# Kernel optimization log

Hardware: AMD Instinct MI355X
Metric: run time of the kernel (lower is better)

The kernel has to match this reference:

```python
import jax, jax.numpy as jnp
import numpy as np
import math

# ---- constants lifted verbatim from the torch source ----
PMLX = 10; PX = 400; TX = PMLX + PX + PMLX          # txsize = 420
PMLY = 10; PY = 400; TY = PMLY + PY + PMLY          # tysize = 420
CX = TX // 2; CY = TY // 2
EPS0 = 1e-9 / 36 / math.pi
MU0 = 4 * math.pi * 1e-7
C0 = 1.0 / math.sqrt(MU0 * EPS0)
DX = 2.5e-8; DY = 2.5e-8
DT = 0.99 / C0 / math.sqrt((1.0 / DX) ** 2 + (1.0 / DY) ** 2)
EPSR_INF = 5.283
EPS_INF = EPS0 * EPSR_INF
F0 = 5.47e14; BW = 0.1 * F0
T = math.sqrt(2.0) * math.sqrt(math.log(2.0)) / (math.pi * BW)
NSTEPS = 200   # reduced from 16000 for the correctness baseline; same per-step math


def setup_inputs() -> dict:
    # Lorentz (complex-pole) silver model from param(): pole/residue -> a0,a1,b0,b1,b2
    pr, pi_ = -4.8113e12, 6.8512e13
    rr, ri = 4.9581e14, -1.511e18
    a0 = -2.0 * (pr * rr + pi_ * ri)
    a1 = 2.0 * rr
    b0 = pr * pr + pi_ * pi_
    b1 = -2.0 * pr
    b2 = 1.0
    den = b0 * DT * DT + 2 * b1 * DT + 4 * b2
    Ca = np.array([-(2 * b0 * DT * DT - 8 * b2) / den], np.float32)
    Cb = np.array([-(b0 * DT * DT - 2 * b1 * DT + 4 * b2) / den], np.float32)
    Cc = np.array([(2 * a0 * EPS0 * DT + 4 * a1 * EPS0) / den], np.float32)
    Cd = np.array([-(8 * a1 * EPS0) / den], np.float32)
    Ce = np.array([(-2 * a0 * EPS0 * DT + 4 * a1 * EPS0) / den], np.float32)
    temp1 = float(Cc[0])                       # sum over tot_pol = 1 pole
    denom = EPS_INF / DT + 0.5 * temp1
    C1 = np.full((TX + 1, TY + 1), (EPS_INF / DT) / denom, np.float32)
    C2 = np.full((TX + 1, TY + 1), 0.5 / denom, np.float32)
    Cb_dx = np.full((TX + 1, TY + 1), 1.0 / denom / DX, np.float32)
    Cb_dy = np.full((TX + 1, TY + 1), 1.0 / denom / DY, np.float32)
    dbhx = np.full((TX + 1, TY), DT / MU0 / DY, np.float32)   # Hx curl coeff
    dbhy = np.full((TX, TY + 1), DT / MU0 / DX, np.float32)   # Hy curl coeff
    # polynomial-graded PML conductivity profiles (pml_param)
    m = 4
    eta0 = 120.0 * math.pi
    smax = 0.8 * (m + 1) / (eta0 * DX)

    def prof(n, npml, off):
        k = np.arange(n, dtype=np.float64)
        dl = np.clip(npml - k - off, 0.0, None) / npml   # depth into left PML
        dr = np.clip(k + off - (n - 1 - npml), 0.0, None) / npml
        return (smax * (dl ** m + dr ** m)).astype(np.float32)

    sig_ex = prof(TX + 1, PMLX, 0.0)
    sig_ey = prof(TY + 1, PMLY, 0.0)
    sig_hx = prof(TX, PMLX, 0.5)   # H nodes on half-grid
    sig_hy = prof(TY, PMLY, 0.5)
    # Gaussian-modulated sine soft source at the grid center
    t = np.arange(NSTEPS, dtype=np.float64) * DT
    src = (np.exp(-(((t - 4 * T) / T) ** 2)) * np.sin(2 * math.pi * F0 * (t - 4 * T))).astype(np.float32)
    return {
        "src": jnp.asarray(src), "C1": jnp.asarray(C1), "C2": jnp.asarray(C2),
        "Cb_dx": jnp.asarray(Cb_dx), "Cb_dy": jnp.asarray(Cb_dy),
        "dbhx": jnp.asarray(dbhx), "dbhy": jnp.asarray(dbhy),
        "Ca": jnp.asarray(Ca), "Cb": jnp.asarray(Cb), "Cc": jnp.asarray(Cc),
        "Cd": jnp.asarray(Cd), "Ce": jnp.asarray(Ce),
        "sig_ex": jnp.asarray(sig_ex), "sig_ey": jnp.asarray(sig_ey),
        "sig_hx": jnp.asarray(sig_hx), "sig_hy": jnp.asarray(sig_hy),
        "n_steps": NSTEPS,
    }


def reference(src, C1, C2, Cb_dx, Cb_dy, dbhx, dbhy, Ca, Cb, Cc, Cd, Ce,
              sig_ex, sig_ey, sig_hx, sig_hy, n_steps):
    # PML damping factors (exponential time-stepping of the conductive loss)
    de = jnp.exp(-(sig_ex[:, None] + sig_ey[None, :]) * (DT / EPS0))     # (421,421) for Ez
    dhx = jnp.exp(-(sig_ex[:, None] + sig_hy[None, :]) * (DT / MU0))     # (421,420) for Hx
    dhy = jnp.exp(-(sig_hx[:, None] + sig_ey[None, :]) * (DT / MU0))     # (420,421) for Hy
    # PEC outer boundary mask
    mask = jnp.pad(jnp.ones((TX - 1, TY - 1), de.dtype), ((1, 1), (1, 1)))
    ca = Ca[:, None, None]; cb = Cb[:, None, None]; cc = Cc[:, None, None]
    cd = Cd[:, None, None]; ce = Ce[:, None, None]

    def step(carry, s):
        Ez, Eold, Hx, Hy, Jz, Jold = carry
        # H-field Yee updates with PML damping
        Hx = dhx * (Hx - dbhx * (Ez[:, 1:] - Ez[:, :-1]))
        Hy = dhy * (Hy + dbhy * (Ez[1:, :] - Ez[:-1, :]))
        # curls onto Ez nodes (interior), zero-padded at PEC boundary
        curlHy = jnp.pad(Hy[1:, :] - Hy[:-1, :], ((1, 1), (0, 0)))       # (421,421)
        curlHx = jnp.pad(Hx[:, 1:] - Hx[:, :-1], ((0, 0), (1, 1)))       # (421,421)
        # Lorentz ADE dispersion source term (tot_pol summed; Cc*Ez^{n+1} folded into C1/C2/Cb_*)
        Phi = jnp.sum((ca + 1.0) * Jz + cb * Jold + cd * Ez[None] + ce * Eold[None], axis=0)
        Ez_new = mask * de * (C1 * Ez + Cb_dx * curlHy - Cb_dy * curlHx - C2 * Phi)
        Ez_new = Ez_new.at[CX, CY].add(s)                                 # soft point source
        # polarization current recurrence
        Jz_new = ca * Jz + cb * Jold + cc * Ez_new[None] + cd * Ez[None] + ce * Eold[None]
        return (Ez_new, Ez, Hx, Hy, Jz_new, Jz), None

    z = jnp.zeros((TX + 1, TY + 1), src.dtype)
    init = (z, z,
            jnp.zeros((TX + 1, TY), src.dtype),
            jnp.zeros((TX, TY + 1), src.dtype),
            jnp.zeros((1, TX + 1, TY + 1), src.dtype),
            jnp.zeros((1, TX + 1, TY + 1), src.dtype))
    (Ez, _, _, _, _, _), _ = jax.lax.scan(step, init, src[:n_steps])
    return Ez
```

## Files before the change

kernel.cpp:

```cpp
#include <hip/hip_runtime.h>
#include <math.h>

#define NXr 421
#define CXr 210
#define NSTEPS_C 200

#define Bt   16
#define Kt   8
#define EXT  32
#define LROWS (EXT + 2)
#define SPITCH 36
#define NBLK 27
#define NPHASE (NSTEPS_C / Kt)
#define SEED_PHASES 4
#define SEED_STEPS (SEED_PHASES * Kt)

#define PP   448
#define PAD  8
#define CP   (CXr + PAD)
#define FSZ  (PP * PP)

#define SB   (CP - 32)
#define SROWS 66
#define SPITCH2 72

struct PParams {
    float *aEz, *aEo, *aJz, *aJo, *aHx, *aHy;
    float *bEz, *bEo, *bJz, *bJo, *bHx, *bHy;
    const float *dexP, *deyP, *aexP, *aeyP, *ahxP, *ahyP;
    const float *C1a, *C2a, *Cbdxa, *Cbdya;
    const float *Caa, *Cba, *Cca, *Cda, *Cea, *dbhxa, *dbhya;
    const float *src;
};

__global__ void init_kernel(const float* __restrict__ sig_ex,
                            const float* __restrict__ sig_ey,
                            const float* __restrict__ sig_hx,
                            const float* __restrict__ sig_hy,
                            float de_fac, float dh_fac,
                            float* __restrict__ zero_base, int n_zero,
                            float* __restrict__ dexP, float* __restrict__ deyP,
                            float* __restrict__ aexP, float* __restrict__ aeyP,
                            float* __restrict__ ahxP, float* __restrict__ ahyP)
{
    int t = blockIdx.x * blockDim.x + threadIdx.x;
    int stride = gridDim.x * blockDim.x;
    for (int k = t; k < n_zero; k += stride) zero_base[k] = 0.0f;
    if (t < PP) {
        int g = t - PAD;
        dexP[t] = (g >= 1 && g <= NXr - 2) ? expf(-sig_ex[g] * de_fac) : 0.0f;
        deyP[t] = (g >= 1 && g <= NXr - 2) ? expf(-sig_ey[g] * de_fac) : 0.0f;
        aexP[t] = (g >= 0 && g <  NXr)     ? expf(-sig_ex[g] * dh_fac) : 0.0f;
        aeyP[t] = (g >= 0 && g <  NXr)     ? expf(-sig_ey[g] * dh_fac) : 0.0f;
        ahxP[t] = (g >= 0 && g <  NXr - 1) ? expf(-sig_hx[g] * dh_fac) : 0.0f;
        ahyP[t] = (g >= 0 && g <  NXr - 1) ? expf(-sig_hy[g] * dh_fac) : 0.0f;
    }
}

__global__ __launch_bounds__(256, 1)
void seed_kernel(PParams p)
{
    __shared__ __align__(16) float sE[2][SROWS][SPITCH2];

    const int tid = threadIdx.x;
    const int tj = tid & 15, ti = tid >> 4;
    const int li0 = 4 * ti, lj0 = 4 * tj;
    const int r0 = SB + li0, c0 = SB + lj0;

    const float ca = p.Caa[0], cb = p.Cba[0], cc = p.Cca[0];
    const float cd = p.Cda[0], ce = p.Cea[0];
    const float ca1 = ca + 1.0f;
    const float C1 = p.C1a[0], C2 = p.C2a[0];
    const float cbdx = p.Cbdxa[0], cbdy = p.Cbdya[0];
    const float dbhx0 = p.dbhxa[0], dbhy0 = p.dbhya[0];

    float dHx[4][4], dHy[4][4], dE[4][4], dHyU[4], dHxL[4], srcw[4][4];
#pragma unroll
    for (int a = 0; a < 4; ++a)
#pragma unroll
        for (int b = 0; b < 4; ++b) {
            dHx[a][b] = p.aexP[r0 + a] * p.ahyP[c0 + b];
            dHy[a][b] = p.ahxP[r0 + a] * p.aeyP[c0 + b];
            dE[a][b]  = p.dexP[r0 + a] * p.deyP[c0 + b];
            srcw[a][b] = ((r0 + a == CP) && (c0 + b == CP)) ? 1.0f : 0.0f;
        }
    {
        float ahxU = p.ahxP[r0 - 1];
        float ahyL = p.ahyP[c0 - 1];
#pragma unroll
        for (int b = 0; b < 4; ++b) dHyU[b] = ahxU * p.aeyP[c0 + b];
#pragma unroll
        for (int a = 0; a < 4; ++a) dHxL[a] = p.aexP[r0 + a] * ahyL;
    }

    float ez[4][4] = {}, eo[4][4] = {}, jz[4][4] = {}, jo[4][4] = {};
    float hx[4][4] = {}, hy[4][4] = {};
    float hyU[4] = {}, hxL[4] = {};

    {
        float* sp = &sE[0][0][0];
        for (int z = tid; z < 2 * SROWS * SPITCH2; z += 256) sp[z] = 0.0f;
    }
    __syncthreads();

#pragma unroll 2
    for (int s = 0; s < SEED_STEPS; ++s) {
        float sv = p.src[s];
        float (*S)[SPITCH2] = sE[s & 1];
#pragma unroll
        for (int a = 0; a < 4; ++a)
            *(float4*)&S[1 + li0 + a][4 + lj0] =
                make_float4(ez[a][0], ez[a][1], ez[a][2], ez[a][3]);

#pragma unroll
        for (int a = 0; a < 4; ++a)
#pragma unroll
            for (int b = 0; b < 3; ++b)
                hx[a][b] = dHx[a][b] * (hx[a][b] - dbhx0 * (ez[a][b+1] - ez[a][b]));
#pragma unroll
        for (int a = 0; a < 3; ++a)
#pragma unroll
            for (int b = 0; b < 4; ++b)
                hy[a][b] = dHy[a][b] * (hy[a][b] + dbhy0 * (ez[a+1][b] - ez[a][b]));

        __syncthreads();

        float eR[4], eL[4];
#pragma unroll
        for (int a = 0; a < 4; ++a) {
            eR[a] = S[1 + li0 + a][4 + lj0 + 4];
            eL[a] = S[1 + li0 + a][3 + lj0];
        }
        float4 eD = *(float4*)&S[1 + li0 + 4][4 + lj0];
        float4 eU = *(float4*)&S[li0][4 + lj0];
        float eDv[4] = {eD.x, eD.y, eD.z, eD.w};
        float eUv[4] = {eU.x, eU.y, eU.z, eU.w};

#pragma unroll
        for (int a = 0; a < 4; ++a)
            hx[a][3] = dHx[a][3] * (hx[a][3] - dbhx0 * (eR[a] - ez[a][3]));
#pragma unroll
        for (int b = 0; b < 4; ++b)
            hy[3][b] = dHy[3][b] * (hy[3][b] + dbhy0 * (eDv[b] - ez[3][b]));
#pragma unroll
        for (int b = 0; b < 4; ++b)
            hyU[b] = dHyU[b] * (hyU[b] + dbhy0 * (ez[0][b] - eUv[b]));
#pragma unroll
        for (int a = 0; a < 4; ++a)
            hxL[a] = dHxL[a] * (hxL[a] - dbhx0 * (ez[a][0] - eL[a]));

#pragma unroll
        for (int a = 0; a < 4; ++a)
#pragma unroll
            for (int b = 0; b < 4; ++b) {
                float cHyv = hy[a][b] - (a == 0 ? hyU[b] : hy[a-1][b]);
                float cHxv = hx[a][b] - (b == 0 ? hxL[a] : hx[a][b-1]);
                float e = ez[a][b], j = jz[a][b];
                float phi = ca1 * j + cb * jo[a][b] + cd * e + ce * eo[a][b];
                float v1 = fmaf(-C2, phi, C1 * e);
                float v2 = fmaf(cbdx, cHyv, v1);
                float en = dE[a][b] * fmaf(-cbdy, cHxv, v2);
                en = fmaf(srcw[a][b], sv, en);
                float jn = fmaf(cc, en, phi - j);
                eo[a][b] = e;  ez[a][b] = en;
                jo[a][b] = j;  jz[a][b] = jn;
            }
    }

#pragma unroll
    for (int a = 0; a < 4; ++a) {
        int g = (r0 + a) * PP + c0;
        *(float4*)&p.aEz[g] = make_float4(ez[a][0], ez[a][1], ez[a][2], ez[a][3]);
        *(float4*)&p.aEo[g] = make_float4(eo[a][0], eo[a][1], eo[a][2], eo[a][3]);
        *(float4*)&p.aJz[g] = make_float4(jz[a][0], jz[a][1], jz[a][2], jz[a][3]);
        *(float4*)&p.aJo[g] = make_float4(jo[a][0], jo[a][1], jo[a][2], jo[a][3]);
        *(float4*)&p.aHx[g] = make_float4(hx[a][0], hx[a][1], hx[a][2], hx[a][3]);
        *(float4*)&p.aHy[g] = make_float4(hy[a][0], hy[a][1], hy[a][2], hy[a][3]);
    }
}

__global__ __launch_bounds__(256)
void phase_kernel(PParams p, int t, int b0, float* __restrict__ out,
                  int writeOut)
{
    __shared__ __align__(16) float sEz[2][LROWS][SPITCH];

    const int tid = threadIdx.x;
    const int tj = tid & 15, ti = tid >> 4;
    const int li0 = 2 * ti, lj0 = 2 * tj;

    const int gx = (int)gridDim.x;
    int orig = (int)blockIdx.y * gx + (int)blockIdx.x;
    int nwg = gx * gx;
    int q = nwg >> 3, rr = nwg & 7;
    int xcd = orig & 7, k = orig >> 3;
    int nid = (xcd < rr ? xcd * (q + 1) : rr * (q + 1) + (xcd - rr) * q) + k;
    int bx = nid % gx, by = nid / gx;

    const int r0 = (bx + b0) * Bt + li0;
    const int c0 = (by + b0) * Bt + lj0;

    const float ca = p.Caa[0], cb = p.Cba[0], cc = p.Cca[0];
    const float cd = p.Cda[0], ce = p.Cea[0];
    const float ca1 = ca + 1.0f;
    const float C1 = p.C1a[0], C2 = p.C2a[0];
    const float cbdx = p.Cbdxa[0], cbdy = p.Cbdya[0];
    const float dbhx0 = p.dbhxa[0], dbhy0 = p.dbhya[0];

    float dHx[2][2], dHy[2][2], dE[2][2], dHyU[2], dHxL[2];
    float srcw[2][2];
#pragma unroll
    for (int a = 0; a < 2; ++a)
#pragma unroll
        for (int b = 0; b < 2; ++b) {
            dHx[a][b] = p.aexP[r0 + a] * p.ahyP[c0 + b];
            dHy[a][b] = p.ahxP[r0 + a] * p.aeyP[c0 + b];
            dE[a][b]  = p.dexP[r0 + a] * p.deyP[c0 + b];
            srcw[a][b] = ((r0 + a == CP) && (c0 + b == CP)) ? 1.0f : 0.0f;
        }
    {
        float ahxU = (r0 > 0) ? p.ahxP[r0 - 1] : 0.0f;
        float ahyL = (c0 > 0) ? p.ahyP[c0 - 1] : 0.0f;
        dHyU[0] = ahxU * p.aeyP[c0];
        dHyU[1] = ahxU * p.aeyP[c0 + 1];
        dHxL[0] = p.aexP[r0] * ahyL;
        dHxL[1] = p.aexP[r0 + 1] * ahyL;
    }

    const bool odd = (t & 1) != 0;
    const float* cEz = odd ? p.bEz : p.aEz;
    const float* cEo = odd ? p.bEo : p.aEo;
    const float* cJz = odd ? p.bJz : p.aJz;
    const float* cJo = odd ? p.bJo : p.aJo;
    const float* cHx = odd ? p.bHx : p.aHx;
    const float* cHy = odd ? p.bHy : p.aHy;
    float* nEz = odd ? p.aEz : p.bEz;
    float* nEo = odd ? p.aEo : p.bEo;
    float* nJz = odd ? p.aJz : p.bJz;
    float* nJo = odd ? p.aJo : p.bJo;
    float* nHx = odd ? p.aHx : p.bHx;
    float* nHy = odd ? p.aHy : p.bHy;

    {
        float* sp = &sEz[0][0][0];
        for (int z = tid; z < 2 * LROWS * SPITCH; z += 256) sp[z] = 0.0f;
    }

    float ez[2][2], eo[2][2], jz[2][2], jo[2][2], hx[2][2], hy[2][2];
#pragma unroll
    for (int a = 0; a < 2; ++a) {
        int g = (r0 + a) * PP + c0;
        float2 v;
        v = *(const float2*)&cEz[g]; ez[a][0] = v.x; ez[a][1] = v.y;
        v = *(const float2*)&cEo[g]; eo[a][0] = v.x; eo[a][1] = v.y;
        v = *(const float2*)&cJz[g]; jz[a][0] = v.x; jz[a][1] = v.y;
        v = *(const float2*)&cJo[g]; jo[a][0] = v.x; jo[a][1] = v.y;
        v = *(const float2*)&cHx[g]; hx[a][0] = v.x; hx[a][1] = v.y;
        v = *(const float2*)&cHy[g]; hy[a][0] = v.x; hy[a][1] = v.y;
    }
    float hyU[2], hxL[2];
    {
        float2 v = *(const float2*)&cHy[(r0 - 1) * PP + c0];
        hyU[0] = v.x; hyU[1] = v.y;
        hxL[0] = cHx[r0 * PP + c0 - 1];
        hxL[1] = cHx[(r0 + 1) * PP + c0 - 1];
    }

    const int n0 = t * Kt;
    float svl[Kt];
#pragma unroll
    for (int s = 0; s < Kt; ++s) svl[s] = p.src[n0 + s];

    __syncthreads();

    for (int s = 0; s < Kt; ++s) {
        float (*S)[SPITCH] = sEz[s & 1];
        *(float2*)&S[1 + li0][2 + lj0] = make_float2(ez[0][0], ez[0][1]);
        *(float2*)&S[2 + li0][2 + lj0] = make_float2(ez[1][0], ez[1][1]);

        hx[0][0] = dHx[0][0] * (hx[0][0] - dbhx0 * (ez[0][1] - ez[0][0]));
        hx[1][0] = dHx[1][0] * (hx[1][0] - dbhx0 * (ez[1][1] - ez[1][0]));
        hy[0][0] = dHy[0][0] * (hy[0][0] + dbhy0 * (ez[1][0] - ez[0][0]));
        hy[0][1] = dHy[0][1] * (hy[0][1] + dbhy0 * (ez[1][1] - ez[0][1]));

        float base[2][2], pj[2][2];
#pragma unroll
        for (int a = 0; a < 2; ++a)
#pragma unroll
            for (int b = 0; b < 2; ++b) {
                float e = ez[a][b], j = jz[a][b];
                float phi = ca1 * j + cb * jo[a][b] + cd * e + ce * eo[a][b];
                base[a][b] = fmaf(-C2, phi, C1 * e);
                pj[a][b] = phi - j;
            }

        __syncthreads();

        float eR0 = S[1 + li0][4 + lj0];
        float eR1 = S[2 + li0][4 + lj0];
        float2 eD = *(float2*)&S[3 + li0][2 + lj0];
        float2 eU = *(float2*)&S[li0][2 + lj0];
        float eL0 = S[1 + li0][1 + lj0];
        float eL1 = S[2 + li0][1 + lj0];

        hx[0][1] = dHx[0][1] * (hx[0][1] - dbhx0 * (eR0 - ez[0][1]));
        hx[1][1] = dHx[1][1] * (hx[1][1] - dbhx0 * (eR1 - ez[1][1]));
        hy[1][0] = dHy[1][0] * (hy[1][0] + dbhy0 * (eD.x - ez[1][0]));
        hy[1][1] = dHy[1][1] * (hy[1][1] + dbhy0 * (eD.y - ez[1][1]));

        hyU[0] = dHyU[0] * (hyU[0] + dbhy0 * (ez[0][0] - eU.x));
        hyU[1] = dHyU[1] * (hyU[1] + dbhy0 * (ez[0][1] - eU.y));
        hxL[0] = dHxL[0] * (hxL[0] - dbhx0 * (ez[0][0] - eL0));
        hxL[1] = dHxL[1] * (hxL[1] - dbhx0 * (ez[1][0] - eL1));

        float sv = svl[s];
        float cHyv[2][2], cHxv[2][2];
        cHyv[0][0] = hy[0][0] - hyU[0];   cHxv[0][0] = hx[0][0] - hxL[0];
        cHyv[0][1] = hy[0][1] - hyU[1];   cHxv[0][1] = hx[0][1] - hx[0][0];
        cHyv[1][0] = hy[1][0] - hy[0][0]; cHxv[1][0] = hx[1][0] - hxL[1];
        cHyv[1][1] = hy[1][1] - hy[0][1]; cHxv[1][1] = hx[1][1] - hx[1][0];

#pragma unroll
        for (int a = 0; a < 2; ++a)
#pragma unroll
            for (int b = 0; b < 2; ++b) {
                float v1 = fmaf(cbdx, cHyv[a][b], base[a][b]);
                float v2 = fmaf(-cbdy, cHxv[a][b], v1);
                float en = dE[a][b] * v2;
                en = fmaf(srcw[a][b], sv, en);
                float jn = fmaf(cc, en, pj[a][b]);
                eo[a][b] = ez[a][b];  ez[a][b] = en;
                jo[a][b] = jz[a][b];  jz[a][b] = jn;
            }
    }

    if (ti >= 4 && ti < 12 && tj >= 4 && tj < 12) {
#pragma unroll
        for (int a = 0; a < 2; ++a) {
            int g = (r0 + a) * PP + c0;
            *(float2*)&nEz[g] = make_float2(ez[a][0], ez[a][1]);
            *(float2*)&nEo[g] = make_float2(eo[a][0], eo[a][1]);
            *(float2*)&nJz[g] = make_float2(jz[a][0], jz[a][1]);
            *(float2*)&nJo[g] = make_float2(jo[a][0], jo[a][1]);
            *(float2*)&nHx[g] = make_float2(hx[a][0], hx[a][1]);
            *(float2*)&nHy[g] = make_float2(hy[a][0], hy[a][1]);
        }
        if (writeOut) {
#pragma unroll
            for (int a = 0; a < 2; ++a)
#pragma unroll
                for (int b = 0; b < 2; ++b) {
                    int gi = r0 + a - PAD, gj = c0 + b - PAD;
                    if (gi < NXr && gj < NXr)
                        out[gi * NXr + gj] = ez[a][b];
                }
        }
    }
}

extern "C" void kernel_launch(void* const* d_in, const int* in_sizes, int n_in,
                              void* d_out, int out_size, void* d_ws, size_t ws_size,
                              hipStream_t stream)
{
    const float* src    = (const float*)d_in[0];
    const float* C1     = (const float*)d_in[1];
    const float* C2     = (const float*)d_in[2];
    const float* Cb_dx  = (const float*)d_in[3];
    const float* Cb_dy  = (const float*)d_in[4];
    const float* dbhx   = (const float*)d_in[5];
    const float* dbhy   = (const float*)d_in[6];
    const float* Ca     = (const float*)d_in[7];
    const float* Cb     = (const float*)d_in[8];
    const float* Cc     = (const float*)d_in[9];
    const float* Cd     = (const float*)d_in[10];
    const float* Ce     = (const float*)d_in[11];
    const float* sig_ex = (const float*)d_in[12];
    const float* sig_ey = (const float*)d_in[13];
    const float* sig_hx = (const float*)d_in[14];
    const float* sig_hy = (const float*)d_in[15];

    const double EPS0 = 1e-9 / 36.0 / M_PI;
    const double MU0  = 4.0 * M_PI * 1e-7;
    const double C0   = 1.0 / sqrt(MU0 * EPS0);
    const double DXd  = 2.5e-8, DYd = 2.5e-8;
    const double DT   = 0.99 / C0 / sqrt(1.0 / (DXd * DXd) + 1.0 / (DYd * DYd));
    const float de_fac = (float)(DT / EPS0);
    const float dh_fac = (float)(DT / MU0);

    float* base = (float*)d_ws;
    float* fields = base + PP;
    float* w = fields + 12 * (size_t)FSZ;
    float* dexP = w; w += PP;
    float* deyP = w; w += PP;
    float* aexP = w; w += PP;
    float* aeyP = w; w += PP;
    float* ahxP = w; w += PP;
    float* ahyP = w; w += PP;

    PParams p;
    p.aEz = fields + 0 * (size_t)FSZ;  p.aEo = fields + 1 * (size_t)FSZ;
    p.aJz = fields + 2 * (size_t)FSZ;  p.aJo = fields + 3 * (size_t)FSZ;
    p.aHx = fields + 4 * (size_t)FSZ;  p.aHy = fields + 5 * (size_t)FSZ;
    p.bEz = fields + 6 * (size_t)FSZ;  p.bEo = fields + 7 * (size_t)FSZ;
    p.bJz = fields + 8 * (size_t)FSZ;  p.bJo = fields + 9 * (size_t)FSZ;
    p.bHx = fields + 10 * (size_t)FSZ; p.bHy = fields + 11 * (size_t)FSZ;
    p.dexP = dexP; p.deyP = deyP; p.aexP = aexP; p.aeyP = aeyP;
    p.ahxP = ahxP; p.ahyP = ahyP;
    p.C1a = C1; p.C2a = C2; p.Cbdxa = Cb_dx; p.Cbdya = Cb_dy;
    p.Caa = Ca; p.Cba = Cb; p.Cca = Cc; p.Cda = Cd; p.Cea = Ce;
    p.dbhxa = dbhx; p.dbhya = dbhy;
    p.src = src;

    init_kernel<<<512, 256, 0, stream>>>(sig_ex, sig_ey, sig_hx, sig_hy,
                                         de_fac, dh_fac,
                                         base, PP + 12 * FSZ,
                                         dexP, deyP, aexP, aeyP, ahxP, ahyP);

    seed_kernel<<<1, 256, 0, stream>>>(p);

    dim3 blk(256);
    for (int t = SEED_PHASES; t < NPHASE; ++t) {
        int R  = 8 * t + 11;
        int lo = CP - R, hi = CP + R;
        int b0 = (lo - (EXT - 1)) / 16; if (b0 < 0) b0 = 0;
        int b1 = hi / 16;               if (b1 > NBLK - 1) b1 = NBLK - 1;
        dim3 g(b1 - b0 + 1, b1 - b0 + 1);
        phase_kernel<<<g, blk, 0, stream>>>(p, t, b0, (float*)d_out,
                                            (t == NPHASE - 1) ? 1 : 0);
    }
}
```

Baseline: 258.1 us.

## Use larger 64x64 temporally-blocked tiles with 16 steps per launch

Each thread now owns a 4x4 cell patch instead of 2x2, so a 256-thread block covers a 64x64 extended tile with a 32x32 output core. It runs 16 time steps per launch instead of 8, which halves the number of phase launches and the global round-trips of the six field arrays. Padding and the phase schedule change to match, with a final 8-step launch. In exchange each thread holds far more registers, which forces one block per CU via launch bounds and lowers occupancy, and the halo recomputation per tile goes up.

```diff
diff --git a/kernel.cpp b/kernel.cpp
--- a/kernel.cpp
+++ b/kernel.cpp
@@ -5,24 +5,20 @@
 #define CXr 210
 #define NSTEPS_C 200
 
-#define Bt   16
-#define Kt   8
-#define EXT  32
-#define LROWS (EXT + 2)
-#define SPITCH 36
-#define NBLK 27
-#define NPHASE (NSTEPS_C / Kt)
-#define SEED_PHASES 4
-#define SEED_STEPS (SEED_PHASES * Kt)
-
-#define PP   448
-#define PAD  8
+#define Bt   32
+#define Kt   16
+#define EXT  64
+#define NBLK 14
+#define SROWS 66
+#define SPITCH2 72
+
+#define PP   480
+#define PAD  16
 #define CP   (CXr + PAD)
 #define FSZ  (PP * PP)
 
 #define SB   (CP - 32)
-#define SROWS 66
-#define SPITCH2 72
+#define SEED_STEPS 32
 
 struct PParams {
     float *aEz, *aEo, *aJz, *aJo, *aHx, *aHy;
@@ -179,22 +175,22 @@
     }
 }
 
-__global__ __launch_bounds__(256)
+__global__ __launch_bounds__(256, 1)
 void phase_kernel(PParams p, int t, int b0, float* __restrict__ out,
-                  int writeOut)
+                  int writeOut, int sN)
 {
-    __shared__ __align__(16) float sEz[2][LROWS][SPITCH];
+    __shared__ __align__(16) float sE[2][SROWS][SPITCH2];
 
     const int tid = threadIdx.x;
     const int tj = tid & 15, ti = tid >> 4;
-    const int li0 = 2 * ti, lj0 = 2 * tj;
+    const int li0 = 4 * ti, lj0 = 4 * tj;
 
     const int gx = (int)gridDim.x;
     int orig = (int)blockIdx.y * gx + (int)blockIdx.x;
     int nwg = gx * gx;
     int q = nwg >> 3, rr = nwg & 7;
-    int xcd = orig & 7, k = orig >> 3;
-    int nid = (xcd < rr ? xcd * (q + 1) : rr * (q + 1) + (xcd - rr) * q) + k;
+    int xcd = orig & 7, kk = orig >> 3;
+    int nid = (xcd < rr ? xcd * (q + 1) : rr * (q + 1) + (xcd - rr) * q) + kk;
     int bx = nid % gx, by = nid / gx;
 
     const int r0 = (bx + b0) * Bt + li0;
@@ -207,12 +203,11 @@
     const float cbdx = p.Cbdxa[0], cbdy = p.Cbdya[0];
     const float dbhx0 = p.dbhxa[0], dbhy0 = p.dbhya[0];
 
-    float dHx[2][2], dHy[2][2], dE[2][2], dHyU[2], dHxL[2];
-    float srcw[2][2];
-#pragma unroll
-    for (int a = 0; a < 2; ++a)
-#pragma unroll
-        for (int b = 0; b < 2; ++b) {
+    float dHx[4][4], dHy[4][4], dE[4][4], dHyU[4], dHxL[4], srcw[4][4];
+#pragma unroll
+    for (int a = 0; a < 4; ++a)
+#pragma unroll
+        for (int b = 0; b < 4; ++b) {
             dHx[a][b] = p.aexP[r0 + a] * p.ahyP[c0 + b];
             dHy[a][b] = p.ahxP[r0 + a] * p.aeyP[c0 + b];
             dE[a][b]  = p.dexP[r0 + a] * p.deyP[c0 + b];
@@ -221,10 +216,10 @@
     {
         float ahxU = (r0 > 0) ? p.ahxP[r0 - 1] : 0.0f;
         float ahyL = (c0 > 0) ? p.ahyP[c0 - 1] : 0.0f;
-        dHyU[0] = ahxU * p.aeyP[c0];
-        dHyU[1] = ahxU * p.aeyP[c0 + 1];
-        dHxL[0] = p.aexP[r0] * ahyL;
-        dHxL[1] = p.aexP[r0 + 1] * ahyL;
+#pragma unroll
+        for (int b = 0; b < 4; ++b) dHyU[b] = ahxU * p.aeyP[c0 + b];
+#pragma unroll
+        for (int a = 0; a < 4; ++a) dHxL[a] = p.aexP[r0 + a] * ahyL;
     }
 
     const bool odd = (t & 1) != 0;
@@ -242,114 +237,123 @@
     float* nHy = odd ? p.aHy : p.bHy;
 
     {
-        float* sp = &sEz[0][0][0];
-        for (int z = tid; z < 2 * LROWS * SPITCH; z += 256) sp[z] = 0.0f;
-    }
-
-    float ez[2][2], eo[2][2], jz[2][2], jo[2][2], hx[2][2], hy[2][2];
-#pragma unroll
-    for (int a = 0; a < 2; ++a) {
+        float* sp = &sE[0][0][0];
+        for (int z = tid; z < 2 * SROWS * SPITCH2; z += 256) sp[z] = 0.0f;
+    }
+
+    float ez[4][4], eo[4][4], jz[4][4], jo[4][4], hx[4][4], hy[4][4];
+#pragma unroll
+    for (int a = 0; a < 4; ++a) {
         int g = (r0 + a) * PP + c0;
-        float2 v;
-        v = *(const float2*)&cEz[g]; ez[a][0] = v.x; ez[a][1] = v.y;
-        v = *(const float2*)&cEo[g]; eo[a][0] = v.x; eo[a][1] = v.y;
-        v = *(const float2*)&cJz[g]; jz[a][0] = v.x; jz[a][1] = v.y;
-        v = *(const float2*)&cJo[g]; jo[a][0] = v.x; jo[a][1] = v.y;
-        v = *(const float2*)&cHx[g]; hx[a][0] = v.x; hx[a][1] = v.y;
-        v = *(const float2*)&cHy[g]; hy[a][0] = v.x; hy[a][1] = v.y;
-    }
-    float hyU[2], hxL[2];
+        float4 v;
+        v = *(const float4*)&cEz[g];
+        ez[a][0]=v.x; ez[a][1]=v.y; ez[a][2]=v.z; ez[a][3]=v.w;
+        v = *(const float4*)&cEo[g];
+        eo[a][0]=v.x; eo[a][1]=v.y; eo[a][2]=v.z; eo[a][3]=v.w;
+        v = *(const float4*)&cJz[g];
+        jz[a][0]=v.x; jz[a][1]=v.y; jz[a][2]=v.z; jz[a][3]=v.w;
+        v = *(const float4*)&cJo[g];
+        jo[a][0]=v.x; jo[a][1]=v.y; jo[a][2]=v.z; jo[a][3]=v.w;
+        v = *(const float4*)&cHx[g];
+        hx[a][0]=v.x; hx[a][1]=v.y; hx[a][2]=v.z; hx[a][3]=v.w;
+        v = *(const float4*)&cHy[g];
+        hy[a][0]=v.x; hy[a][1]=v.y; hy[a][2]=v.z; hy[a][3]=v.w;
+    }
+    float hyU[4], hxL[4];
     {
-        float2 v = *(const float2*)&cHy[(r0 - 1) * PP + c0];
-        hyU[0] = v.x; hyU[1] = v.y;
-        hxL[0] = cHx[r0 * PP + c0 - 1];
-        hxL[1] = cHx[(r0 + 1) * PP + c0 - 1];
-    }
-
-    const int n0 = t * Kt;
-    float svl[Kt];
-#pragma unroll
-    for (int s = 0; s < Kt; ++s) svl[s] = p.src[n0 + s];
+        float4 v = *(const float4*)&cHy[(r0 - 1) * PP + c0];
+        hyU[0]=v.x; hyU[1]=v.y; hyU[2]=v.z; hyU[3]=v.w;
+#pragma unroll
+        for (int a = 0; a < 4; ++a)
+            hxL[a] = cHx[(r0 + a) * PP + c0 - 1];
+    }
+
+    const int n0 = 32 + 16 * t;
 
     __syncthreads();
 
-    for (int s = 0; s < Kt; ++s) {
-        float (*S)[SPITCH] = sEz[s & 1];
-        *(float2*)&S[1 + li0][2 + lj0] = make_float2(ez[0][0], ez[0][1]);
-        *(float2*)&S[2 + li0][2 + lj0] = make_float2(ez[1][0], ez[1][1]);
-
-        hx[0][0] = dHx[0][0] * (hx[0][0] - dbhx0 * (ez[0][1] - ez[0][0]));
-        hx[1][0] = dHx[1][0] * (hx[1][0] - dbhx0 * (ez[1][1] - ez[1][0]));
-        hy[0][0] = dHy[0][0] * (hy[0][0] + dbhy0 * (ez[1][0] - ez[0][0]));
-        hy[0][1] = dHy[0][1] * (hy[0][1] + dbhy0 * (ez[1][1] - ez[0][1]));
-
-        float base[2][2], pj[2][2];
-#pragma unroll
-        for (int a = 0; a < 2; ++a)
-#pragma unroll
-            for (int b = 0; b < 2; ++b) {
+    auto step = [&](float (*S)[SPITCH2], float sv) {
+#pragma unroll
+        for (int a = 0; a < 4; ++a)
+            *(float4*)&S[1 + li0 + a][4 + lj0] =
+                make_float4(ez[a][0], ez[a][1], ez[a][2], ez[a][3]);
+
+#pragma unroll
+        for (int a = 0; a < 4; ++a)
+#pragma unroll
+            for (int b = 0; b < 3; ++b)
+                hx[a][b] = dHx[a][b] * (hx[a][b] - dbhx0 * (ez[a][b+1] - ez[a][b]));
+#pragma unroll
+        for (int a = 0; a < 3; ++a)
+#pragma unroll
+            for (int b = 0; b < 4; ++b)
+                hy[a][b] = dHy[a][b] * (hy[a][b] + dbhy0 * (ez[a+1][b] - ez[a][b]));
+
+        __syncthreads();
+
+        float eR[4], eL[4];
+#pragma unroll
+        for (int a = 0; a < 4; ++a) {
+            eR[a] = S[1 + li0 + a][4 + lj0 + 4];
+            eL[a] = S[1 + li0 + a][3 + lj0];
+        }
+        float4 eD = *(float4*)&S[1 + li0 + 4][4 + lj0];
+        float4 eU = *(float4*)&S[li0][4 + lj0];
+        float eDv[4] = {eD.x, eD.y, eD.z, eD.w};
+        float eUv[4] = {eU.x, eU.y, eU.z, eU.w};
+
+#pragma unroll
+        for (int a = 0; a < 4; ++a)
+            hx[a][3] = dHx[a][3] * (hx[a][3] - dbhx0 * (eR[a] - ez[a][3]));
+#pragma unroll
+        for (int b = 0; b < 4; ++b)
+            hy[3][b] = dHy[3][b] * (hy[3][b] + dbhy0 * (eDv[b] - ez[3][b]));
+#pragma unroll
+        for (int b = 0; b < 4; ++b)
+            hyU[b] = dHyU[b] * (hyU[b] + dbhy0 * (ez[0][b] - eUv[b]));
+#pragma unroll
+        for (int a = 0; a < 4; ++a)
+            hxL[a] = dHxL[a] * (hxL[a] - dbhx0 * (ez[a][0] - eL[a]));
+
+#pragma unroll
+        for (int a = 0; a < 4; ++a)
+#pragma unroll
+            for (int b = 0; b < 4; ++b) {
+                float cHyv = hy[a][b] - (a == 0 ? hyU[b] : hy[a-1][b]);
+                float cHxv = hx[a][b] - (b == 0 ? hxL[a] : hx[a][b-1]);
                 float e = ez[a][b], j = jz[a][b];
                 float phi = ca1 * j + cb * jo[a][b] + cd * e + ce * eo[a][b];
-                base[a][b] = fmaf(-C2, phi, C1 * e);
-                pj[a][b] = phi - j;
+                float v1 = fmaf(-C2, phi, C1 * e);
+                float v2 = fmaf(cbdx, cHyv, v1);
+                float en = dE[a][b] * fmaf(-cbdy, cHxv, v2);
+                en = fmaf(srcw[a][b], sv, en);
+                float jn = fmaf(cc, en, phi - j);
+                eo[a][b] = e;  ez[a][b] = en;
+                jo[a][b] = j;  jz[a][b] = jn;
             }
-
-        __syncthreads();
-
-        float eR0 = S[1 + li0][4 + lj0];
-        float eR1 = S[2 + li0][4 + lj0];
-        float2 eD = *(float2*)&S[3 + li0][2 + lj0];
-        float2 eU = *(float2*)&S[li0][2 + lj0];
-        float eL0 = S[1 + li0][1 + lj0];
-        float eL1 = S[2 + li0][1 + lj0];
-
-        hx[0][1] = dHx[0][1] * (hx[0][1] - dbhx0 * (eR0 - ez[0][1]));
-        hx[1][1] = dHx[1][1] * (hx[1][1] - dbhx0 * (eR1 - ez[1][1]));
-        hy[1][0] = dHy[1][0] * (hy[1][0] + dbhy0 * (eD.x - ez[1][0]));
-        hy[1][1] = dHy[1][1] * (hy[1][1] + dbhy0 * (eD.y - ez[1][1]));
-
-        hyU[0] = dHyU[0] * (hyU[0] + dbhy0 * (ez[0][0] - eU.x));
-        hyU[1] = dHyU[1] * (hyU[1] + dbhy0 * (ez[0][1] - eU.y));
-        hxL[0] = dHxL[0] * (hxL[0] - dbhx0 * (ez[0][0] - eL0));
-        hxL[1] = dHxL[1] * (hxL[1] - dbhx0 * (ez[1][0] - eL1));
-
-        float sv = svl[s];
-        float cHyv[2][2], cHxv[2][2];
-        cHyv[0][0] = hy[0][0] - hyU[0];   cHxv[0][0] = hx[0][0] - hxL[0];
-        cHyv[0][1] = hy[0][1] - hyU[1];   cHxv[0][1] = hx[0][1] - hx[0][0];
-        cHyv[1][0] = hy[1][0] - hy[0][0]; cHxv[1][0] = hx[1][0] - hxL[1];
-        cHyv[1][1] = hy[1][1] - hy[0][1]; cHxv[1][1] = hx[1][1] - hx[1][0];
-
-#pragma unroll
-        for (int a = 0; a < 2; ++a)
-#pragma unroll
-            for (int b = 0; b < 2; ++b) {
-                float v1 = fmaf(cbdx, cHyv[a][b], base[a][b]);
-                float v2 = fmaf(-cbdy, cHxv[a][b], v1);
-                float en = dE[a][b] * v2;
-                en = fmaf(srcw[a][b], sv, en);
-                float jn = fmaf(cc, en, pj[a][b]);
-                eo[a][b] = ez[a][b];  ez[a][b] = en;
-                jo[a][b] = jz[a][b];  jz[a][b] = jn;
-            }
+    };
+
+    for (int ss = 0; ss < sN; ss += 2) {
+        step(sE[0], p.src[n0 + ss]);
+        step(sE[1], p.src[n0 + ss + 1]);
     }
 
     if (ti >= 4 && ti < 12 && tj >= 4 && tj < 12) {
 #pragma unroll
-        for (int a = 0; a < 2; ++a) {
+        for (int a = 0; a < 4; ++a) {
             int g = (r0 + a) * PP + c0;
-            *(float2*)&nEz[g] = make_float2(ez[a][0], ez[a][1]);
-            *(float2*)&nEo[g] = make_float2(eo[a][0], eo[a][1]);
-            *(float2*)&nJz[g] = make_float2(jz[a][0], jz[a][1]);
-            *(float2*)&nJo[g] = make_float2(jo[a][0], jo[a][1]);
-            *(float2*)&nHx[g] = make_float2(hx[a][0], hx[a][1]);
-            *(float2*)&nHy[g] = make_float2(hy[a][0], hy[a][1]);
+            *(float4*)&nEz[g] = make_float4(ez[a][0], ez[a][1], ez[a][2], ez[a][3]);
+            *(float4*)&nEo[g] = make_float4(eo[a][0], eo[a][1], eo[a][2], eo[a][3]);
+            *(float4*)&nJz[g] = make_float4(jz[a][0], jz[a][1], jz[a][2], jz[a][3]);
+            *(float4*)&nJo[g] = make_float4(jo[a][0], jo[a][1], jo[a][2], jo[a][3]);
+            *(float4*)&nHx[g] = make_float4(hx[a][0], hx[a][1], hx[a][2], hx[a][3]);
+            *(float4*)&nHy[g] = make_float4(hy[a][0], hy[a][1], hy[a][2], hy[a][3]);
         }
         if (writeOut) {
 #pragma unroll
-            for (int a = 0; a < 2; ++a)
-#pragma unroll
-                for (int b = 0; b < 2; ++b) {
+            for (int a = 0; a < 4; ++a)
+#pragma unroll
+                for (int b = 0; b < 4; ++b) {
                     int gi = r0 + a - PAD, gj = c0 + b - PAD;
                     if (gi < NXr && gj < NXr)
                         out[gi * NXr + gj] = ez[a][b];
@@ -419,13 +423,14 @@
     seed_kernel<<<1, 256, 0, stream>>>(p);
 
     dim3 blk(256);
-    for (int t = SEED_PHASES; t < NPHASE; ++t) {
-        int R  = 8 * t + 11;
+    for (int i = 0; i <= 10; ++i) {
+        int sN = (i == 10) ? 8 : 16;
+        int R  = 16 * i + 51;
         int lo = CP - R, hi = CP + R;
-        int b0 = (lo - (EXT - 1)) / 16; if (b0 < 0) b0 = 0;
-        int b1 = hi / 16;               if (b1 > NBLK - 1) b1 = NBLK - 1;
+        int b0 = (lo - (EXT - 1)) / Bt; if (b0 < 0) b0 = 0;
+        int b1 = hi / Bt;               if (b1 > NBLK - 1) b1 = NBLK - 1;
         dim3 g(b1 - b0 + 1, b1 - b0 + 1);
-        phase_kernel<<<g, blk, 0, stream>>>(p, t, b0, (float*)d_out,
-                                            (t == NPHASE - 1) ? 1 : 0);
+        phase_kernel<<<g, blk, 0, stream>>>(p, i, b0, (float*)d_out,
+                                            (i == 10) ? 1 : 0, sN);
     }
 }
```

Measured after the change: 282.9 us. +9.6%, slower.
